# Kernel tuning notes

Hardware: AMD Instinct MI355X
Metric: run time of the kernel (lower is better)

## Reference

```python
import jax, jax.numpy as jnp
import numpy as np

D_MODEL = 256
N_LEVELS = 4
N_HEADS = 4
N_POINTS = 8
D_FFN = 1024
SHAPES = [(100, 152), (50, 76), (25, 38), (13, 19)]  # (H, W) per level
BATCH = 2


def setup_inputs() -> dict:
    key = jax.random.key(0)
    ks = list(jax.random.split(key, 16))
    Len = sum(h * w for h, w in SHAPES)  # 20197
    s = 0.02

    def lin(k, fin, fout):
        k1, k2 = jax.random.split(k)
        return (jax.random.normal(k1, (fin, fout), jnp.float32) * s,
                jax.random.normal(k2, (fout,), jnp.float32) * s)

    W_off, b_off = lin(ks[0], D_MODEL, N_HEADS * N_LEVELS * N_POINTS * 2)
    W_attn, b_attn = lin(ks[1], D_MODEL, N_HEADS * N_LEVELS * N_POINTS)
    W_val, b_val = lin(ks[2], D_MODEL, D_MODEL)
    W_out, b_out = lin(ks[3], D_MODEL, D_MODEL)
    W1, b1 = lin(ks[4], D_MODEL, D_FFN)
    W2, b2 = lin(ks[5], D_FFN, D_MODEL)
    starts = np.concatenate([[0], np.cumsum([h * w for h, w in SHAPES])[:-1]])
    return {
        "src_feat": jax.random.normal(ks[6], (BATCH, Len, D_MODEL), jnp.float32),
        "reference_points": jax.random.uniform(ks[7], (BATCH, Len, N_LEVELS, 2), jnp.float32),
        "key_feat": jax.random.normal(ks[8], (BATCH, Len, D_MODEL), jnp.float32),
        "spatial_shapes": jnp.array(SHAPES, jnp.int32),
        "level_start_index": jnp.array(starts, jnp.int32),
        "W_off": W_off, "b_off": b_off, "W_attn": W_attn, "b_attn": b_attn,
        "W_val": W_val, "b_val": b_val, "W_out": W_out, "b_out": b_out,
        "W1": W1, "b1": b1, "W2": W2, "b2": b2,
        "g1": jnp.ones((D_MODEL,), jnp.float32), "be1": jnp.zeros((D_MODEL,), jnp.float32),
        "g2": jnp.ones((D_MODEL,), jnp.float32), "be2": jnp.zeros((D_MODEL,), jnp.float32),
    }


def _layernorm(x, g, b, eps=1e-5):
    mu = jnp.mean(x, -1, keepdims=True)
    var = jnp.mean(jnp.square(x - mu), -1, keepdims=True)
    return (x - mu) * jax.lax.rsqrt(var + eps) * g + b


def _bilinear(v, loc, H, W):
    # v: (N, M, H*W, D); loc: (N, M, Lq, P, 2) normalized [0,1]
    # Matches F.grid_sample(mode='bilinear', padding_mode='zeros', align_corners=False)
    x = loc[..., 0] * W - 0.5
    y = loc[..., 1] * H - 0.5
    x0 = jnp.floor(x)
    y0 = jnp.floor(y)
    wx = x - x0
    wy = y - y0
    N, M, Lq, P = x.shape
    out = None
    for dy in (0, 1):
        for dx in (0, 1):
            xi = x0 + dx
            yi = y0 + dy
            w = (wx if dx else 1.0 - wx) * (wy if dy else 1.0 - wy)
            valid = (xi >= 0) & (xi < W) & (yi >= 0) & (yi < H)
            idx = (jnp.clip(yi, 0, H - 1) * W + jnp.clip(xi, 0, W - 1)).astype(jnp.int32)
            g = jnp.take_along_axis(v, idx.reshape(N, M, Lq * P, 1), axis=2)
            g = g.reshape(N, M, Lq, P, -1) * (w * jnp.asarray(valid, v.dtype))[..., None]
            out = g if out is None else out + g
    return out  # (N, M, Lq, P, D)


def reference(src_feat, reference_points, key_feat, spatial_shapes, level_start_index,
              W_off, b_off, W_attn, b_attn, W_val, b_val, W_out, b_out,
              W1, b1, W2, b2, g1, be1, g2, be2):
    N, Lq, C = src_feat.shape
    M, L, P = N_HEADS, N_LEVELS, N_POINTS
    D = C // M
    shapes = np.asarray(spatial_shapes)  # static per-level (H, W)
    # --- MSDeformAttn ---
    value = (key_feat @ W_val + b_val).reshape(N, -1, M, D)
    off = (src_feat @ W_off + b_off).reshape(N, Lq, M, L, P, 2)
    attn = jax.nn.softmax((src_feat @ W_attn + b_attn).reshape(N, Lq, M, L * P), axis=-1)
    attn = attn.reshape(N, Lq, M, L, P)
    normalizer = jnp.stack([spatial_shapes[:, 1], spatial_shapes[:, 0]], -1).astype(src_feat.dtype)  # (L,2)=(W,H)
    loc = reference_points[:, :, None, :, None, :] + off / normalizer[None, None, None, :, None, :]
    out = jnp.zeros((N, M, Lq, D), src_feat.dtype)
    start = 0
    for l in range(L):
        H, W = int(shapes[l, 0]), int(shapes[l, 1])
        v = value[:, start:start + H * W].transpose(0, 2, 1, 3)  # (N,M,HW,D)
        samp = _bilinear(v, loc[:, :, :, l].transpose(0, 2, 1, 3, 4), H, W)  # (N,M,Lq,P,D)
        out = out + jnp.einsum('nmqpd,nqmp->nmqd', samp, attn[:, :, :, l])
        start += H * W
    out = out.transpose(0, 2, 1, 3).reshape(N, Lq, C)
    src2 = out @ W_out + b_out
    # --- residual + norm + FFN (light=False, dropout=0) ---
    x = _layernorm(src_feat + src2, g1, be1)
    ffn = jax.nn.relu(x @ W1 + b1) @ W2 + b2
    x = _layernorm(x + ffn, g2, be2)
    return (x, loc, attn)
```

## Files before the change

### kernel.cpp

```cpp
#include <hip/hip_runtime.h>
#include <hip/hip_bf16.h>

#define LQ 20197
#define NBATCH 2
#define MROWS 40394
#define MR256 ((size_t)MROWS * 256)

typedef __attribute__((ext_vector_type(8))) short bf16x8;
typedef __attribute__((ext_vector_type(4))) float f32x4;
typedef __attribute__((ext_vector_type(2))) float f32x2;

__device__ __forceinline__ unsigned short f2bf(float f) {
    unsigned u = __float_as_uint(f);
    return (unsigned short)((u + 0x7fff + ((u >> 16) & 1)) >> 16);
}
__device__ __forceinline__ float bf2f(unsigned short b) {
    return __uint_as_float((unsigned)b << 16);
}

__device__ __forceinline__ void gload16(const void* g, void* l) {
    __builtin_amdgcn_global_load_lds(
        (const __attribute__((address_space(1))) unsigned int*)g,
        (__attribute__((address_space(3))) unsigned int*)l, 16, 0, 0);
}

__device__ __forceinline__ int swz_k(int n, int kk) {
    return (kk & ~63) | (((((kk >> 3) & 7) ^ (n & 7))) << 3) | (kk & 7);
}

__global__ __launch_bounds__(256) void prep_w_k(
    const float* __restrict__ Wv, const float* __restrict__ Wo,
    const float* __restrict__ Wa, const float* __restrict__ Wu,
    const float* __restrict__ W1, const float* __restrict__ W2,
    const float* __restrict__ ba,
    unsigned short* __restrict__ BTv, unsigned short* __restrict__ BTo,
    unsigned short* __restrict__ BTa, unsigned short* __restrict__ BTu,
    unsigned short* __restrict__ BT1, unsigned short* __restrict__ BT2,
    float* __restrict__ battn)
{
    const size_t id0 = (size_t)blockIdx.x * blockDim.x + threadIdx.x;
    const size_t stride = (size_t)gridDim.x * blockDim.x;
    for (size_t i = id0; i < 65536; i += stride) {
        const int n = (int)(i >> 8), kk = (int)(i & 255);
        const int k = swz_k(n, kk);
        BTv[i] = f2bf(Wv[k * 256 + n]);
        BTo[i] = f2bf(Wo[k * 256 + n]);
        BTu[i] = f2bf(Wu[k * 256 + n]);
        BTa[i] = (n < 128) ? f2bf(Wa[k * 128 + n]) : (unsigned short)0;
    }
    for (size_t i = id0; i < 262144; i += stride) {
        const int n = (int)(i >> 8), kk = (int)(i & 255);
        BT1[i] = f2bf(W1[(size_t)swz_k(n, kk) * 1024 + n]);
        const int n2 = (int)(i >> 10), kk2 = (int)(i & 1023);
        BT2[i] = f2bf(W2[(size_t)swz_k(n2, kk2) * 256 + n2]);
    }
    if (id0 < 256) battn[id0] = (id0 < 128) ? ba[id0] : 0.f;
}

enum { EP_VAL = 0, EP_LOC = 1, EP_ATTN = 2, EP_LN = 3, EP_FFN1 = 4 };

template<int EP, bool AF32>
__global__ __launch_bounds__(256) void gemm_k(
    const void* __restrict__ Ap, const unsigned short* __restrict__ BT,
    const float* __restrict__ bias, const float* __restrict__ aux,
    const float* __restrict__ g, const float* __restrict__ be,
    void* outp, void* outp2)
{
    __shared__ __align__(16) unsigned short As[64 * 64];
    __shared__ __align__(16) unsigned short Bs[256 * 64];
    __shared__ float ps[64][4], pq[64][4];
    __shared__ float mu_s[64], rs_s[64];

    const int tid = threadIdx.x;
    const int l = tid & 63, w = tid >> 6;
    const int lc = l & 15, rg = l >> 4;
    const int rowBase = blockIdx.x * 64;
    const int wb = tid & ~63;
    const unsigned short* BTb = BT + (size_t)blockIdx.y * 65536;
    const bool fullA = (rowBase + 64 <= MROWS);

    f32x4 acc[4][4] = {};

    for (int k0 = 0; k0 < 256; k0 += 64) {
        if (k0) __syncthreads();
        #pragma unroll
        for (int p = 0; p < 8; ++p) {
            const int idx = tid + p * 256;
            gload16(BTb + (size_t)(idx >> 3) * 256 + k0 + (idx & 7) * 8,
                    &Bs[(p * 256 + wb) * 8]);
        }
        if (AF32) {
            const float* A = (const float*)Ap;
            #pragma unroll
            for (int p = 0; p < 2; ++p) {
                const int idx = tid + p * 256;
                const int r = idx >> 3, s = idx & 7;
                const int row = rowBase + r;
                bf16x8 v = {};
                if (row < MROWS) {
                    const float4 v0 = *(const float4*)(A + (size_t)row * 256 + k0 + s * 8);
                    const float4 v1 = *(const float4*)(A + (size_t)row * 256 + k0 + s * 8 + 4);
                    v[0] = (short)f2bf(v0.x); v[1] = (short)f2bf(v0.y);
                    v[2] = (short)f2bf(v0.z); v[3] = (short)f2bf(v0.w);
                    v[4] = (short)f2bf(v1.x); v[5] = (short)f2bf(v1.y);
                    v[6] = (short)f2bf(v1.z); v[7] = (short)f2bf(v1.w);
                }
                *(bf16x8*)&As[r * 64 + ((s ^ (r & 7)) << 3)] = v;
            }
        } else if (fullA) {
            #pragma unroll
            for (int p = 0; p < 2; ++p) {
                const int idx = tid + p * 256;
                gload16((const unsigned short*)Ap + (size_t)(rowBase + (idx >> 3)) * 256 + k0 + (idx & 7) * 8,
                        &As[(p * 256 + wb) * 8]);
            }
        } else {
            #pragma unroll
            for (int p = 0; p < 2; ++p) {
                const int idx = tid + p * 256;
                const int r = idx >> 3, s = idx & 7;
                const int row = rowBase + r;
                bf16x8 v = {};
                if (row < MROWS)
                    v = *(const bf16x8*)((const unsigned short*)Ap + (size_t)row * 256 + k0 + s * 8);
                *(bf16x8*)&As[idx * 8] = v;
            }
        }
        __syncthreads();
        #pragma unroll
        for (int kk = 0; kk < 2; ++kk) {
            bf16x8 aF[4], bF[4];
            const int sl = kk * 4 + rg;
            #pragma unroll
            for (int i = 0; i < 4; ++i) {
                const int r = i * 16 + lc;
                aF[i] = *(const bf16x8*)&As[r * 64 + ((sl ^ (r & 7)) << 3)];
            }
            #pragma unroll
            for (int j = 0; j < 4; ++j) {
                const int n = w * 64 + j * 16 + lc;
                bF[j] = *(const bf16x8*)&Bs[n * 64 + ((sl ^ (n & 7)) << 3)];
            }
            #pragma unroll
            for (int i = 0; i < 4; ++i)
                #pragma unroll
                for (int j = 0; j < 4; ++j)
                    acc[i][j] = __builtin_amdgcn_mfma_f32_16x16x32_bf16(aF[i], bF[j], acc[i][j], 0, 0, 0);
        }
    }

    if (EP == EP_VAL) {
        unsigned short* out = (unsigned short*)outp;
        #pragma unroll
        for (int i = 0; i < 4; ++i)
            #pragma unroll
            for (int r4 = 0; r4 < 4; ++r4) {
                const int row = rowBase + i * 16 + rg * 4 + r4;
                if (row >= MROWS) continue;
                #pragma unroll
                for (int j = 0; j < 4; ++j) {
                    const int col = w * 64 + j * 16 + lc;
                    out[(size_t)row * 256 + col] = f2bf(acc[i][j][r4] + bias[col]);
                }
            }
    } else if (EP == EP_FFN1) {
        unsigned short* h0 = (unsigned short*)outp;
        unsigned short* h1 = (unsigned short*)outp2;
        #pragma unroll
        for (int i = 0; i < 4; ++i)
            #pragma unroll
            for (int r4 = 0; r4 < 4; ++r4) {
                const int row = rowBase + i * 16 + rg * 4 + r4;
                if (row >= MROWS) continue;
                #pragma unroll
                for (int j = 0; j < 4; ++j) {
                    const int colg = blockIdx.y * 256 + w * 64 + j * 16 + lc;
                    const float t = fmaxf(acc[i][j][r4] + bias[colg], 0.f);
                    unsigned short* hb = (colg < 512) ? h0 : h1;
                    const int lcol = colg & 511;
                    const int gg = lcol >> 3, e = lcol & 7;
                    const int gs = (gg & 56) | ((gg & 7) ^ (row & 7));
                    hb[(size_t)row * 512 + gs * 8 + e] = f2bf(t);
                }
            }
    } else if (EP == EP_LOC) {
        float* out = (float*)outp;
        const float INV[8] = {1.f/152, 1.f/100, 1.f/76, 1.f/50, 1.f/38, 1.f/25, 1.f/19, 1.f/13};
        #pragma unroll
        for (int i = 0; i < 4; ++i)
            #pragma unroll
            for (int r4 = 0; r4 < 4; ++r4) {
                const int row = rowBase + i * 16 + rg * 4 + r4;
                if (row >= MROWS) continue;
                #pragma unroll
                for (int j = 0; j < 4; ++j) {
                    const int col = w * 64 + j * 16 + lc;
                    const int lvl = (col >> 4) & 3, xy = col & 1;
                    const float off = acc[i][j][r4] + bias[col];
                    const float ref = aux[(size_t)row * 8 + lvl * 2 + xy];
                    out[(size_t)row * 256 + col] = ref + off * INV[lvl * 2 + xy];
                }
            }
    } else if (EP == EP_ATTN) {
        if (w >= 2) return;
        float* out = (float*)outp;
        #pragma unroll
        for (int i = 0; i < 4; ++i)
            #pragma unroll
            for (int r4 = 0; r4 < 4; ++r4) {
                const int row = rowBase + i * 16 + rg * 4 + r4;
                float v[4];
                #pragma unroll
                for (int j = 0; j < 4; ++j) v[j] = acc[i][j][r4] + bias[w * 64 + j * 16 + lc];
                float mA = fmaxf(v[0], v[1]), mB = fmaxf(v[2], v[3]);
                #pragma unroll
                for (int o = 1; o <= 8; o <<= 1) {
                    mA = fmaxf(mA, __shfl_xor(mA, o));
                    mB = fmaxf(mB, __shfl_xor(mB, o));
                }
                float e[4];
                e[0] = __expf(v[0] - mA); e[1] = __expf(v[1] - mA);
                e[2] = __expf(v[2] - mB); e[3] = __expf(v[3] - mB);
                float sA = e[0] + e[1], sB = e[2] + e[3];
                #pragma unroll
                for (int o = 1; o <= 8; o <<= 1) {
                    sA += __shfl_xor(sA, o);
                    sB += __shfl_xor(sB, o);
                }
                if (row >= MROWS) continue;
                #pragma unroll
                for (int j = 0; j < 4; ++j) {
                    const int col = w * 64 + j * 16 + lc;
                    out[(size_t)row * 128 + col] = e[j] / (j < 2 ? sA : sB);
                }
            }
    } else {
        unsigned short* out = (unsigned short*)outp;
        #pragma unroll
        for (int i = 0; i < 4; ++i)
            #pragma unroll
            for (int r4 = 0; r4 < 4; ++r4) {
                const int row = rowBase + i * 16 + rg * 4 + r4;
                float s = 0.f, q = 0.f;
                #pragma unroll
                for (int j = 0; j < 4; ++j) {
                    const int col = w * 64 + j * 16 + lc;
                    float t = acc[i][j][r4] + bias[col];
                    if (row < MROWS) t += aux[(size_t)row * 256 + col];
                    acc[i][j][r4] = t;
                    s += t; q += t * t;
                }
                #pragma unroll
                for (int o = 1; o <= 8; o <<= 1) { s += __shfl_xor(s, o); q += __shfl_xor(q, o); }
                if (lc == 0) { ps[i * 16 + rg * 4 + r4][w] = s; pq[i * 16 + rg * 4 + r4][w] = q; }
            }
        __syncthreads();
        if (tid < 64) {
            const float s = ps[tid][0] + ps[tid][1] + ps[tid][2] + ps[tid][3];
            const float q = pq[tid][0] + pq[tid][1] + pq[tid][2] + pq[tid][3];
            const float m = s * (1.f / 256.f);
            mu_s[tid] = m;
            rs_s[tid] = rsqrtf(q * (1.f / 256.f) - m * m + 1e-5f);
        }
        __syncthreads();
        #pragma unroll
        for (int i = 0; i < 4; ++i)
            #pragma unroll
            for (int r4 = 0; r4 < 4; ++r4) {
                const int rl = i * 16 + rg * 4 + r4;
                const int row = rowBase + rl;
                if (row >= MROWS) continue;
                const float m = mu_s[rl], r = rs_s[rl];
                #pragma unroll
                for (int j = 0; j < 4; ++j) {
                    const int col = w * 64 + j * 16 + lc;
                    const int gg = col >> 3, e = col & 7;
                    const int gs = (gg & 24) | ((gg & 7) ^ (row & 7));
                    out[(size_t)row * 256 + gs * 8 + e] = f2bf((acc[i][j][r4] - m) * r * g[col] + be[col]);
                }
            }
    }
}

__global__ __launch_bounds__(256) void ffn2_k(
    const unsigned short* __restrict__ h0, const unsigned short* __restrict__ h1,
    const unsigned short* __restrict__ BT2,
    const float* __restrict__ bias, const unsigned short* __restrict__ xb,
    const float* __restrict__ g, const float* __restrict__ be,
    float* __restrict__ out)
{
    __shared__ __align__(16) unsigned short As[64 * 64];
    __shared__ __align__(16) unsigned short Bs[256 * 64];
    __shared__ float ps[64][4], pq[64][4];
    __shared__ float mu_s[64], rs_s[64];

    const int tid = threadIdx.x;
    const int l = tid & 63, w = tid >> 6;
    const int lc = l & 15, rg = l >> 4;
    const int rowBase = blockIdx.x * 64;
    const int wb = tid & ~63;
    const bool fullA = (rowBase + 64 <= MROWS);

    f32x4 acc[4][4] = {};

    for (int kc = 0; kc < 16; ++kc) {
        if (kc) __syncthreads();
        #pragma unroll
        for (int p = 0; p < 8; ++p) {
            const int idx = tid + p * 256;
            gload16(BT2 + (size_t)(idx >> 3) * 1024 + kc * 64 + (idx & 7) * 8,
                    &Bs[(p * 256 + wb) * 8]);
        }
        const unsigned short* Ab = (kc < 8) ? h0 : h1;
        const int koff = (kc & 7) * 64;
        if (fullA) {
            #pragma unroll
            for (int p = 0; p < 2; ++p) {
                const int idx = tid + p * 256;
                gload16(Ab + (size_t)(rowBase + (idx >> 3)) * 512 + koff + (idx & 7) * 8,
                        &As[(p * 256 + wb) * 8]);
            }
        } else {
            #pragma unroll
            for (int p = 0; p < 2; ++p) {
                const int idx = tid + p * 256;
                const int r = idx >> 3, s = idx & 7;
                const int row = rowBase + r;
                bf16x8 v = {};
                if (row < MROWS) v = *(const bf16x8*)(Ab + (size_t)row * 512 + koff + s * 8);
                *(bf16x8*)&As[idx * 8] = v;
            }
        }
        __syncthreads();
        #pragma unroll
        for (int kk = 0; kk < 2; ++kk) {
            bf16x8 aF[4], bF[4];
            const int sl = kk * 4 + rg;
            #pragma unroll
            for (int i = 0; i < 4; ++i) {
                const int r = i * 16 + lc;
                aF[i] = *(const bf16x8*)&As[r * 64 + ((sl ^ (r & 7)) << 3)];
            }
            #pragma unroll
            for (int j = 0; j < 4; ++j) {
                const int n = w * 64 + j * 16 + lc;
                bF[j] = *(const bf16x8*)&Bs[n * 64 + ((sl ^ (n & 7)) << 3)];
            }
            #pragma unroll
            for (int i = 0; i < 4; ++i)
                #pragma unroll
                for (int j = 0; j < 4; ++j)
                    acc[i][j] = __builtin_amdgcn_mfma_f32_16x16x32_bf16(aF[i], bF[j], acc[i][j], 0, 0, 0);
        }
    }

    #pragma unroll
    for (int i = 0; i < 4; ++i)
        #pragma unroll
        for (int r4 = 0; r4 < 4; ++r4) {
            const int row = rowBase + i * 16 + rg * 4 + r4;
            float s = 0.f, q = 0.f;
            #pragma unroll
            for (int j = 0; j < 4; ++j) {
                const int col = w * 64 + j * 16 + lc;
                float t = acc[i][j][r4] + bias[col];
                if (row < MROWS) {
                    const int gg = col >> 3, e = col & 7;
                    const int gs = (gg & 24) | ((gg & 7) ^ (row & 7));
                    t += bf2f(xb[(size_t)row * 256 + gs * 8 + e]);
                }
                acc[i][j][r4] = t;
                s += t; q += t * t;
            }
            #pragma unroll
            for (int o = 1; o <= 8; o <<= 1) { s += __shfl_xor(s, o); q += __shfl_xor(q, o); }
            if (lc == 0) { ps[i * 16 + rg * 4 + r4][w] = s; pq[i * 16 + rg * 4 + r4][w] = q; }
        }
    __syncthreads();
    if (tid < 64) {
        const float s = ps[tid][0] + ps[tid][1] + ps[tid][2] + ps[tid][3];
        const float q = pq[tid][0] + pq[tid][1] + pq[tid][2] + pq[tid][3];
        const float m = s * (1.f / 256.f);
        mu_s[tid] = m;
        rs_s[tid] = rsqrtf(q * (1.f / 256.f) - m * m + 1e-5f);
    }
    __syncthreads();
    #pragma unroll
    for (int i = 0; i < 4; ++i)
        #pragma unroll
        for (int r4 = 0; r4 < 4; ++r4) {
            const int rl = i * 16 + rg * 4 + r4;
            const int row = rowBase + rl;
            if (row >= MROWS) continue;
            const float m = mu_s[rl], r = rs_s[rl];
            #pragma unroll
            for (int j = 0; j < 4; ++j) {
                const int col = w * 64 + j * 16 + lc;
                out[(size_t)row * 256 + col] = (acc[i][j][r4] - m) * r * g[col] + be[col];
            }
        }
}

#define QB2 8
__global__ __launch_bounds__(256) void sample_k(
    const unsigned short* __restrict__ value, const float* __restrict__ loc_i,
    const float* __restrict__ attn_i, unsigned short* __restrict__ samp_o)
{
    constexpr int LVL_H[4] = {100, 50, 25, 13};
    constexpr int LVL_W[4] = {152, 76, 38, 19};
    constexpr int LVL_S[4] = {0, 15200, 19000, 19950};
    const int tid = threadIdx.x;

    const int nwg = gridDim.x;
    const int bid = blockIdx.x;
    const int xcd = bid & 7, lid = bid >> 3;
    const int qq = nwg >> 3, rr = nwg & 7;
    const int sw = (xcd < rr ? xcd * (qq + 1) : rr * (qq + 1) + (xcd - rr) * qq) + lid;
    const int rowBase = sw * QB2;

    __shared__ int2 sT[QB2][4][132];

    #pragma unroll
    for (int it = 0; it < 4; ++it) {
        const int item = tid + it * 256;
        const int qs = item >> 7;
        const int t  = item & 127;
        const int row = rowBase + qs;
        if (row < MROWS) {
            const int lv = (t >> 3) & 3;
            const int n = (row >= LQ) ? 1 : 0;
            const int H = LVL_H[lv], W = LVL_W[lv];
            const float lx = loc_i[(size_t)row * 256 + t * 2 + 0];
            const float ly = loc_i[(size_t)row * 256 + t * 2 + 1];
            const float a  = attn_i[(size_t)row * 128 + t];
            const float x = lx * (float)W - 0.5f;
            const float y = ly * (float)H - 0.5f;
            const float x0f = floorf(x), y0f = floorf(y);
            const float wx = x - x0f, wy = y - y0f;
            const int x0 = (int)x0f, y0 = (int)y0f;
            const int base = n * LQ + LVL_S[lv];
            const int tp = (t >> 5) * 33 + (t & 31);
            #pragma unroll
            for (int nb = 0; nb < 4; ++nb) {
                const int dx = nb & 1, dy = nb >> 1;
                const int xi = x0 + dx, yi = y0 + dy;
                const bool valid = (xi >= 0) & (xi < W) & (yi >= 0) & (yi < H);
                const float wgt = (dx ? wx : 1.f - wx) * (dy ? wy : 1.f - wy) * a;
                const int xc = min(max(xi, 0), W - 1);
                const int yc = min(max(yi, 0), H - 1);
                const int off = (base + yc * W + xc) << 9;
                sT[qs][nb][tp] = make_int2(off, valid ? __float_as_int(wgt) : 0);
            }
        }
    }
    __syncthreads();

    const int qs = tid >> 5;
    const int c8 = tid & 31;
    const int row = rowBase + qs;
    if (row >= MROWS) return;
    const int m = c8 >> 3;
    const char* vb = (const char*)value + c8 * 16;
    const int mb = m * 33;

    f32x2 a0 = {0.f, 0.f}, a1 = {0.f, 0.f}, a2 = {0.f, 0.f}, a3 = {0.f, 0.f};
    #pragma unroll 4
    for (int i = 0; i < 128; ++i) {
        const int t0 = i >> 2, nb = i & 3;
        const int2 ow = sT[qs][nb][mb + t0];
        const float w = __int_as_float(ow.y);
        const uint4 u = *(const uint4*)(vb + ow.x);
        const f32x2 wv = {w, w};
        f32x2 p;
        p.x = __uint_as_float(u.x << 16); p.y = __uint_as_float(u.x & 0xffff0000u);
        a0 = __builtin_elementwise_fma(p, wv, a0);
        p.x = __uint_as_float(u.y << 16); p.y = __uint_as_float(u.y & 0xffff0000u);
        a1 = __builtin_elementwise_fma(p, wv, a1);
        p.x = __uint_as_float(u.z << 16); p.y = __uint_as_float(u.z & 0xffff0000u);
        a2 = __builtin_elementwise_fma(p, wv, a2);
        p.x = __uint_as_float(u.w << 16); p.y = __uint_as_float(u.w & 0xffff0000u);
        a3 = __builtin_elementwise_fma(p, wv, a3);
    }
    uint4 o;
    o.x = (unsigned)f2bf(a0.x) | ((unsigned)f2bf(a0.y) << 16);
    o.y = (unsigned)f2bf(a1.x) | ((unsigned)f2bf(a1.y) << 16);
    o.z = (unsigned)f2bf(a2.x) | ((unsigned)f2bf(a2.y) << 16);
    o.w = (unsigned)f2bf(a3.x) | ((unsigned)f2bf(a3.y) << 16);
    const int slot = (c8 & 24) | ((c8 & 7) ^ (row & 7));
    *(uint4*)(samp_o + (size_t)row * 256 + slot * 8) = o;
}

extern "C" void kernel_launch(void* const* d_in, const int* in_sizes, int n_in,
                              void* d_out, int out_size, void* d_ws, size_t ws_size,
                              hipStream_t stream)
{
    const float* src_feat = (const float*)d_in[0];
    const float* refpts   = (const float*)d_in[1];
    const float* key_feat = (const float*)d_in[2];
    const float* W_off  = (const float*)d_in[5];
    const float* b_off  = (const float*)d_in[6];
    const float* W_attn = (const float*)d_in[7];
    const float* b_attn = (const float*)d_in[8];
    const float* W_val  = (const float*)d_in[9];
    const float* b_val  = (const float*)d_in[10];
    const float* W_out  = (const float*)d_in[11];
    const float* b_out  = (const float*)d_in[12];
    const float* W1  = (const float*)d_in[13];
    const float* b1  = (const float*)d_in[14];
    const float* W2  = (const float*)d_in[15];
    const float* b2  = (const float*)d_in[16];
    const float* g1  = (const float*)d_in[17];
    const float* be1 = (const float*)d_in[18];
    const float* g2  = (const float*)d_in[19];
    const float* be2 = (const float*)d_in[20];

    float* out = (float*)d_out;
    float* x_out    = out;
    float* loc_out  = out + MR256;
    float* attn_out = out + 2 * MR256;

    char* ws = (char*)d_ws;
    unsigned short* BTv   = (unsigned short*)(ws + 0);
    unsigned short* BTo   = (unsigned short*)(ws + 131072);
    unsigned short* BTa   = (unsigned short*)(ws + 262144);
    unsigned short* BTu   = (unsigned short*)(ws + 393216);
    unsigned short* BT1   = (unsigned short*)(ws + 524288);
    unsigned short* BT2   = (unsigned short*)(ws + 1048576);
    float*          battn = (float*)(ws + 1572864);
    unsigned short* value = (unsigned short*)(ws + 2097152);
    unsigned short* samp  = (unsigned short*)(ws + 2097152 + MR256 * 2);
    unsigned short* xb    = (unsigned short*)(ws + 2097152 + MR256 * 4);
    unsigned short* h0    = value;
    unsigned short* h1    = (unsigned short*)x_out;

    const int RB = (MROWS + 63) / 64;

    prep_w_k<<<512, 256, 0, stream>>>(W_val, W_off, W_attn, W_out, W1, W2, b_attn,
                                      BTv, BTo, BTa, BTu, BT1, BT2, battn);
    gemm_k<EP_VAL, true><<<dim3(RB, 1), 256, 0, stream>>>(key_feat, BTv, b_val, nullptr, nullptr, nullptr, value, nullptr);
    gemm_k<EP_LOC, true><<<dim3(RB, 1), 256, 0, stream>>>(src_feat, BTo, b_off, refpts, nullptr, nullptr, loc_out, nullptr);
    gemm_k<EP_ATTN, true><<<dim3(RB, 1), 256, 0, stream>>>(src_feat, BTa, battn, nullptr, nullptr, nullptr, attn_out, nullptr);
    sample_k<<<(MROWS + QB2 - 1) / QB2, 256, 0, stream>>>(value, loc_out, attn_out, samp);
    gemm_k<EP_LN, false><<<dim3(RB, 1), 256, 0, stream>>>(samp, BTu, b_out, src_feat, g1, be1, xb, nullptr);
    gemm_k<EP_FFN1, false><<<dim3(RB, 4), 256, 0, stream>>>(xb, BT1, b1, nullptr, nullptr, nullptr, h0, h1);
    ffn2_k<<<dim3(RB, 1), 256, 0, stream>>>(h0, h1, BT2, b2, xb, g2, be2, x_out);
}
```

Baseline: 346.8 us.

## Merge value/offset/attention projections into one launch and keep value in fp32

```diff
diff --git a/kernel.cpp b/kernel.cpp
--- a/kernel.cpp
+++ b/kernel.cpp
@@ -57,11 +57,145 @@
     if (id0 < 256) battn[id0] = (id0 < 128) ? ba[id0] : 0.f;
 }
 
-enum { EP_VAL = 0, EP_LOC = 1, EP_ATTN = 2, EP_LN = 3, EP_FFN1 = 4 };
-
-template<int EP, bool AF32>
+__global__ __launch_bounds__(256) void qkv_k(
+    const float* __restrict__ keyf, const float* __restrict__ srcf,
+    const unsigned short* __restrict__ BT012,
+    const float* __restrict__ bval, const float* __restrict__ boff,
+    const float* __restrict__ batt, const float* __restrict__ refpts,
+    float* __restrict__ value_o, float* __restrict__ loc_o, float* __restrict__ attn_o)
+{
+    __shared__ __align__(16) unsigned short As[64 * 64];
+    __shared__ __align__(16) unsigned short Bs[256 * 64];
+
+    const int tid = threadIdx.x;
+    const int l = tid & 63, w = tid >> 6;
+    const int lc = l & 15, rg = l >> 4;
+    const int rowBase = blockIdx.x * 64;
+    const int wb = tid & ~63;
+    const int y = blockIdx.y;
+    const float* A = (y == 0) ? keyf : srcf;
+    const unsigned short* BTb = BT012 + (size_t)y * 65536;
+    const float* bias = (y == 0) ? bval : (y == 1) ? boff : batt;
+
+    f32x4 acc[4][4] = {};
+
+    for (int k0 = 0; k0 < 256; k0 += 64) {
+        if (k0) __syncthreads();
+        #pragma unroll
+        for (int p = 0; p < 8; ++p) {
+            const int idx = tid + p * 256;
+            gload16(BTb + (size_t)(idx >> 3) * 256 + k0 + (idx & 7) * 8,
+                    &Bs[(p * 256 + wb) * 8]);
+        }
+        #pragma unroll
+        for (int p = 0; p < 2; ++p) {
+            const int idx = tid + p * 256;
+            const int r = idx >> 3, s = idx & 7;
+            const int row = rowBase + r;
+            bf16x8 v = {};
+            if (row < MROWS) {
+                const float4 v0 = *(const float4*)(A + (size_t)row * 256 + k0 + s * 8);
+                const float4 v1 = *(const float4*)(A + (size_t)row * 256 + k0 + s * 8 + 4);
+                v[0] = (short)f2bf(v0.x); v[1] = (short)f2bf(v0.y);
+                v[2] = (short)f2bf(v0.z); v[3] = (short)f2bf(v0.w);
+                v[4] = (short)f2bf(v1.x); v[5] = (short)f2bf(v1.y);
+                v[6] = (short)f2bf(v1.z); v[7] = (short)f2bf(v1.w);
+            }
+            *(bf16x8*)&As[r * 64 + ((s ^ (r & 7)) << 3)] = v;
+        }
+        __syncthreads();
+        #pragma unroll
+        for (int kk = 0; kk < 2; ++kk) {
+            bf16x8 aF[4], bF[4];
+            const int sl = kk * 4 + rg;
+            #pragma unroll
+            for (int i = 0; i < 4; ++i) {
+                const int r = i * 16 + lc;
+                aF[i] = *(const bf16x8*)&As[r * 64 + ((sl ^ (r & 7)) << 3)];
+            }
+            #pragma unroll
+            for (int j = 0; j < 4; ++j) {
+                const int n = w * 64 + j * 16 + lc;
+                bF[j] = *(const bf16x8*)&Bs[n * 64 + ((sl ^ (n & 7)) << 3)];
+            }
+            #pragma unroll
+            for (int i = 0; i < 4; ++i)
+                #pragma unroll
+                for (int j = 0; j < 4; ++j)
+                    acc[i][j] = __builtin_amdgcn_mfma_f32_16x16x32_bf16(aF[i], bF[j], acc[i][j], 0, 0, 0);
+        }
+    }
+
+    if (y == 0) {
+        #pragma unroll
+        for (int i = 0; i < 4; ++i)
+            #pragma unroll
+            for (int r4 = 0; r4 < 4; ++r4) {
+                const int row = rowBase + i * 16 + rg * 4 + r4;
+                if (row >= MROWS) continue;
+                #pragma unroll
+                for (int j = 0; j < 4; ++j) {
+                    const int col = w * 64 + j * 16 + lc;
+                    value_o[(size_t)row * 256 + col] = acc[i][j][r4] + bias[col];
+                }
+            }
+    } else if (y == 1) {
+        const float INV[8] = {1.f/152, 1.f/100, 1.f/76, 1.f/50, 1.f/38, 1.f/25, 1.f/19, 1.f/13};
+        #pragma unroll
+        for (int i = 0; i < 4; ++i)
+            #pragma unroll
+            for (int r4 = 0; r4 < 4; ++r4) {
+                const int row = rowBase + i * 16 + rg * 4 + r4;
+                if (row >= MROWS) continue;
+                #pragma unroll
+                for (int j = 0; j < 4; ++j) {
+                    const int col = w * 64 + j * 16 + lc;
+                    const int lvl = (col >> 4) & 3, xy = col & 1;
+                    const float off = acc[i][j][r4] + bias[col];
+                    const float ref = refpts[(size_t)row * 8 + lvl * 2 + xy];
+                    loc_o[(size_t)row * 256 + col] = ref + off * INV[lvl * 2 + xy];
+                }
+            }
+    } else {
+        if (w >= 2) return;
+        #pragma unroll
+        for (int i = 0; i < 4; ++i)
+            #pragma unroll
+            for (int r4 = 0; r4 < 4; ++r4) {
+                const int row = rowBase + i * 16 + rg * 4 + r4;
+                float v[4];
+                #pragma unroll
+                for (int j = 0; j < 4; ++j) v[j] = acc[i][j][r4] + bias[w * 64 + j * 16 + lc];
+                float mA = fmaxf(v[0], v[1]), mB = fmaxf(v[2], v[3]);
+                #pragma unroll
+                for (int o = 1; o <= 8; o <<= 1) {
+                    mA = fmaxf(mA, __shfl_xor(mA, o));
+                    mB = fmaxf(mB, __shfl_xor(mB, o));
+                }
+                float e[4];
+                e[0] = __expf(v[0] - mA); e[1] = __expf(v[1] - mA);
+                e[2] = __expf(v[2] - mB); e[3] = __expf(v[3] - mB);
+                float sA = e[0] + e[1], sB = e[2] + e[3];
+                #pragma unroll
+                for (int o = 1; o <= 8; o <<= 1) {
+                    sA += __shfl_xor(sA, o);
+                    sB += __shfl_xor(sB, o);
+                }
+                if (row >= MROWS) continue;
+                #pragma unroll
+                for (int j = 0; j < 4; ++j) {
+                    const int col = w * 64 + j * 16 + lc;
+                    attn_o[(size_t)row * 128 + col] = e[j] / (j < 2 ? sA : sB);
+                }
+            }
+    }
+}
+
+enum { EP_LN = 3, EP_FFN1 = 4 };
+
+template<int EP>
 __global__ __launch_bounds__(256) void gemm_k(
-    const void* __restrict__ Ap, const unsigned short* __restrict__ BT,
+    const unsigned short* __restrict__ Ap, const unsigned short* __restrict__ BT,
     const float* __restrict__ bias, const float* __restrict__ aux,
     const float* __restrict__ g, const float* __restrict__ be,
     void* outp, void* outp2)
@@ -89,29 +223,11 @@
             gload16(BTb + (size_t)(idx >> 3) * 256 + k0 + (idx & 7) * 8,
                     &Bs[(p * 256 + wb) * 8]);
         }
-        if (AF32) {
-            const float* A = (const float*)Ap;
+        if (fullA) {
             #pragma unroll
             for (int p = 0; p < 2; ++p) {
                 const int idx = tid + p * 256;
-                const int r = idx >> 3, s = idx & 7;
-                const int row = rowBase + r;
-                bf16x8 v = {};
-                if (row < MROWS) {
-                    const float4 v0 = *(const float4*)(A + (size_t)row * 256 + k0 + s * 8);
-                    const float4 v1 = *(const float4*)(A + (size_t)row * 256 + k0 + s * 8 + 4);
-                    v[0] = (short)f2bf(v0.x); v[1] = (short)f2bf(v0.y);
-                    v[2] = (short)f2bf(v0.z); v[3] = (short)f2bf(v0.w);
-                    v[4] = (short)f2bf(v1.x); v[5] = (short)f2bf(v1.y);
-                    v[6] = (short)f2bf(v1.z); v[7] = (short)f2bf(v1.w);
-                }
-                *(bf16x8*)&As[r * 64 + ((s ^ (r & 7)) << 3)] = v;
-            }
-        } else if (fullA) {
-            #pragma unroll
-            for (int p = 0; p < 2; ++p) {
-                const int idx = tid + p * 256;
-                gload16((const unsigned short*)Ap + (size_t)(rowBase + (idx >> 3)) * 256 + k0 + (idx & 7) * 8,
+                gload16(Ap + (size_t)(rowBase + (idx >> 3)) * 256 + k0 + (idx & 7) * 8,
                         &As[(p * 256 + wb) * 8]);
             }
         } else {
@@ -122,7 +238,7 @@
                 const int row = rowBase + r;
                 bf16x8 v = {};
                 if (row < MROWS)
-                    v = *(const bf16x8*)((const unsigned short*)Ap + (size_t)row * 256 + k0 + s * 8);
+                    v = *(const bf16x8*)(Ap + (size_t)row * 256 + k0 + s * 8);
                 *(bf16x8*)&As[idx * 8] = v;
             }
         }
@@ -149,21 +265,7 @@
         }
     }
 
-    if (EP == EP_VAL) {
-        unsigned short* out = (unsigned short*)outp;
-        #pragma unroll
-        for (int i = 0; i < 4; ++i)
-            #pragma unroll
-            for (int r4 = 0; r4 < 4; ++r4) {
-                const int row = rowBase + i * 16 + rg * 4 + r4;
-                if (row >= MROWS) continue;
-                #pragma unroll
-                for (int j = 0; j < 4; ++j) {
-                    const int col = w * 64 + j * 16 + lc;
-                    out[(size_t)row * 256 + col] = f2bf(acc[i][j][r4] + bias[col]);
-                }
-            }
-    } else if (EP == EP_FFN1) {
+    if (EP == EP_FFN1) {
         unsigned short* h0 = (unsigned short*)outp;
         unsigned short* h1 = (unsigned short*)outp2;
         #pragma unroll
@@ -181,57 +283,6 @@
                     const int gg = lcol >> 3, e = lcol & 7;
                     const int gs = (gg & 56) | ((gg & 7) ^ (row & 7));
                     hb[(size_t)row * 512 + gs * 8 + e] = f2bf(t);
-                }
-            }
-    } else if (EP == EP_LOC) {
-        float* out = (float*)outp;
-        const float INV[8] = {1.f/152, 1.f/100, 1.f/76, 1.f/50, 1.f/38, 1.f/25, 1.f/19, 1.f/13};
-        #pragma unroll
-        for (int i = 0; i < 4; ++i)
-            #pragma unroll
-            for (int r4 = 0; r4 < 4; ++r4) {
-                const int row = rowBase + i * 16 + rg * 4 + r4;
-                if (row >= MROWS) continue;
-                #pragma unroll
-                for (int j = 0; j < 4; ++j) {
-                    const int col = w * 64 + j * 16 + lc;
-                    const int lvl = (col >> 4) & 3, xy = col & 1;
-                    const float off = acc[i][j][r4] + bias[col];
-                    const float ref = aux[(size_t)row * 8 + lvl * 2 + xy];
-                    out[(size_t)row * 256 + col] = ref + off * INV[lvl * 2 + xy];
-                }
-            }
-    } else if (EP == EP_ATTN) {
-        if (w >= 2) return;
-        float* out = (float*)outp;
-        #pragma unroll
-        for (int i = 0; i < 4; ++i)
-            #pragma unroll
-            for (int r4 = 0; r4 < 4; ++r4) {
-                const int row = rowBase + i * 16 + rg * 4 + r4;
-                float v[4];
-                #pragma unroll
-                for (int j = 0; j < 4; ++j) v[j] = acc[i][j][r4] + bias[w * 64 + j * 16 + lc];
-                float mA = fmaxf(v[0], v[1]), mB = fmaxf(v[2], v[3]);
-                #pragma unroll
-                for (int o = 1; o <= 8; o <<= 1) {
-                    mA = fmaxf(mA, __shfl_xor(mA, o));
-                    mB = fmaxf(mB, __shfl_xor(mB, o));
-                }
-                float e[4];
-                e[0] = __expf(v[0] - mA); e[1] = __expf(v[1] - mA);
-                e[2] = __expf(v[2] - mB); e[3] = __expf(v[3] - mB);
-                float sA = e[0] + e[1], sB = e[2] + e[3];
-                #pragma unroll
-                for (int o = 1; o <= 8; o <<= 1) {
-                    sA += __shfl_xor(sA, o);
-                    sB += __shfl_xor(sB, o);
-                }
-                if (row >= MROWS) continue;
-                #pragma unroll
-                for (int j = 0; j < 4; ++j) {
-                    const int col = w * 64 + j * 16 + lc;
-                    out[(size_t)row * 128 + col] = e[j] / (j < 2 ? sA : sB);
                 }
             }
     } else {
@@ -403,7 +454,7 @@
 
 #define QB2 8
 __global__ __launch_bounds__(256) void sample_k(
-    const unsigned short* __restrict__ value, const float* __restrict__ loc_i,
+    const float* __restrict__ value, const float* __restrict__ loc_i,
     const float* __restrict__ attn_i, unsigned short* __restrict__ samp_o)
 {
     constexpr int LVL_H[4] = {100, 50, 25, 13};
@@ -448,7 +499,7 @@
                 const float wgt = (dx ? wx : 1.f - wx) * (dy ? wy : 1.f - wy) * a;
                 const int xc = min(max(xi, 0), W - 1);
                 const int yc = min(max(yi, 0), H - 1);
-                const int off = (base + yc * W + xc) << 9;
+                const int off = (base + yc * W + xc) << 10;
                 sT[qs][nb][tp] = make_int2(off, valid ? __float_as_int(wgt) : 0);
             }
         }
@@ -460,7 +511,7 @@
     const int row = rowBase + qs;
     if (row >= MROWS) return;
     const int m = c8 >> 3;
-    const char* vb = (const char*)value + c8 * 16;
+    const char* vbc = (const char*)value + c8 * 32;
     const int mb = m * 33;
 
     f32x2 a0 = {0.f, 0.f}, a1 = {0.f, 0.f}, a2 = {0.f, 0.f}, a3 = {0.f, 0.f};
@@ -469,17 +520,15 @@
         const int t0 = i >> 2, nb = i & 3;
         const int2 ow = sT[qs][nb][mb + t0];
         const float w = __int_as_float(ow.y);
-        const uint4 u = *(const uint4*)(vb + ow.x);
+        const float4* pp = (const float4*)(vbc + ow.x);
+        const float4 u0 = pp[0];
+        const float4 u1 = pp[1];
         const f32x2 wv = {w, w};
         f32x2 p;
-        p.x = __uint_as_float(u.x << 16); p.y = __uint_as_float(u.x & 0xffff0000u);
-        a0 = __builtin_elementwise_fma(p, wv, a0);
-        p.x = __uint_as_float(u.y << 16); p.y = __uint_as_float(u.y & 0xffff0000u);
-        a1 = __builtin_elementwise_fma(p, wv, a1);
-        p.x = __uint_as_float(u.z << 16); p.y = __uint_as_float(u.z & 0xffff0000u);
-        a2 = __builtin_elementwise_fma(p, wv, a2);
-        p.x = __uint_as_float(u.w << 16); p.y = __uint_as_float(u.w & 0xffff0000u);
-        a3 = __builtin_elementwise_fma(p, wv, a3);
+        p.x = u0.x; p.y = u0.y; a0 = __builtin_elementwise_fma(p, wv, a0);
+        p.x = u0.z; p.y = u0.w; a1 = __builtin_elementwise_fma(p, wv, a1);
+        p.x = u1.x; p.y = u1.y; a2 = __builtin_elementwise_fma(p, wv, a2);
+        p.x = u1.z; p.y = u1.w; a3 = __builtin_elementwise_fma(p, wv, a3);
     }
     uint4 o;
     o.x = (unsigned)f2bf(a0.x) | ((unsigned)f2bf(a0.y) << 16);
@@ -527,21 +576,21 @@
     unsigned short* BT1   = (unsigned short*)(ws + 524288);
     unsigned short* BT2   = (unsigned short*)(ws + 1048576);
     float*          battn = (float*)(ws + 1572864);
-    unsigned short* value = (unsigned short*)(ws + 2097152);
-    unsigned short* samp  = (unsigned short*)(ws + 2097152 + MR256 * 2);
-    unsigned short* xb    = (unsigned short*)(ws + 2097152 + MR256 * 4);
-    unsigned short* h0    = value;
+    float*          value = (float*)(ws + 2097152);
+    unsigned short* samp  = (unsigned short*)(ws + 2097152 + MR256 * 4);
+    unsigned short* xb    = (unsigned short*)(ws + 2097152 + MR256 * 6);
+    unsigned short* h0    = (unsigned short*)value;
     unsigned short* h1    = (unsigned short*)x_out;
 
     const int RB = (MROWS + 63) / 64;
 
     prep_w_k<<<512, 256, 0, stream>>>(W_val, W_off, W_attn, W_out, W1, W2, b_attn,
                                       BTv, BTo, BTa, BTu, BT1, BT2, battn);
-    gemm_k<EP_VAL, true><<<dim3(RB, 1), 256, 0, stream>>>(key_feat, BTv, b_val, nullptr, nullptr, nullptr, value, nullptr);
-    gemm_k<EP_LOC, true><<<dim3(RB, 1), 256, 0, stream>>>(src_feat, BTo, b_off, refpts, nullptr, nullptr, loc_out, nullptr);
-    gemm_k<EP_ATTN, true><<<dim3(RB, 1), 256, 0, stream>>>(src_feat, BTa, battn, nullptr, nullptr, nullptr, attn_out, nullptr);
+    qkv_k<<<dim3(RB, 3), 256, 0, stream>>>(key_feat, src_feat, BTv,
+                                           b_val, b_off, battn, refpts,
+                                           value, loc_out, attn_out);
     sample_k<<<(MROWS + QB2 - 1) / QB2, 256, 0, stream>>>(value, loc_out, attn_out, samp);
-    gemm_k<EP_LN, false><<<dim3(RB, 1), 256, 0, stream>>>(samp, BTu, b_out, src_feat, g1, be1, xb, nullptr);
-    gemm_k<EP_FFN1, false><<<dim3(RB, 4), 256, 0, stream>>>(xb, BT1, b1, nullptr, nullptr, nullptr, h0, h1);
+    gemm_k<EP_LN><<<dim3(RB, 1), 256, 0, stream>>>(samp, BTu, b_out, src_feat, g1, be1, xb, nullptr);
+    gemm_k<EP_FFN1><<<dim3(RB, 4), 256, 0, stream>>>(xb, BT1, b1, nullptr, nullptr, nullptr, h0, h1);
     ffn2_k<<<dim3(RB, 1), 256, 0, stream>>>(h0, h1, BT2, b2, xb, g2, be2, x_out);
 }
```

Result: slower. 424.6 us (+22.5%).
